# Kernel optimization log

Hardware: AMD Instinct MI355X
Metric: run time of the kernel (lower is better)

Reference implementation:

```python
import jax, jax.numpy as jnp
import numpy as np

N = 16384

def setup_inputs() -> dict:
    key = jax.random.key(0)
    k1, k2 = jax.random.split(key)
    predict = jax.random.normal(k1, (N,), dtype=jnp.float32)
    target = jax.random.normal(k2, (N,), dtype=jnp.float32)
    return {"predict": predict, "target": target}

def reference(predict, target):
    n = predict.shape[0]
    # hardtanh(predict[i]-predict[j]) * hardtanh(target[i]-target[j]) summed over i>j.
    # The product matrix is symmetric with zero diagonal, so the strict lower-
    # triangular sum equals half the full-matrix sum.
    pd = jnp.clip(predict[:, None] - predict[None, :], -1.0, 1.0)  # [N, N]
    td = jnp.clip(target[:, None] - target[None, :], -1.0, 1.0)   # [N, N]
    full_sum = jnp.sum(pd * td)
    num = full_sum * 0.5
    denom = jnp.asarray(n * (n - 1), dtype=predict.dtype)
    return 1.0 - 2.0 * num / denom
```

## Files before the change

### kernel.cpp

```cpp
#include <hip/hip_runtime.h>

#define BLOCK 512
#define IPT   4
#define ITILE 2048
#define JS    128
#define JT_PER_I 16
#define NT    576
#define RBLOCK 1024

typedef _Float16 h2 __attribute__((ext_vector_type(2)));

__global__ __launch_bounds__(BLOCK) void kendall_pairs(
    const float* __restrict__ p, const float* __restrict__ t,
    float* __restrict__ partial, int n) {
    __shared__ unsigned int sjp[JS / 2];
    __shared__ unsigned int sjt[JS / 2];

    const int s = blockIdx.x;
    int bi = (int)((__builtin_sqrtf(4.0f + 2.0f * (float)s) - 2.0f) * 0.25f);
    while (8 * (bi + 1) * (bi + 2) <= s) ++bi;
    while (8 * bi * (bi + 1) > s) --bi;
    const int bj = s - 8 * bi * (bi + 1);
    const float w = (bj < JT_PER_I * bi) ? 2.0f : 1.0f;

    if (threadIdx.x < JS) {
        const int k = threadIdx.x & 63;
        const float2* src = (const float2*)((threadIdx.x < 64 ? p : t) + bj * JS);
        float2 v = src[k];
        h2 hv = {(_Float16)v.x, (_Float16)v.y};
        unsigned int bitsv; __builtin_memcpy(&bitsv, &hv, 4);
        (threadIdx.x < 64 ? sjp : sjt)[k] = bitsv;
    }

    h2 pi2[IPT], ti2[IPT];
#pragma unroll
    for (int u = 0; u < IPT; ++u) {
        int i = bi * ITILE + u * BLOCK + threadIdx.x;
        _Float16 ph = (_Float16)p[i];
        _Float16 th = (_Float16)t[i];
        pi2[u] = (h2){ph, ph};
        ti2[u] = (h2){th, th};
    }
    __syncthreads();

    const h2 neg1 = {(_Float16)-1.0f, (_Float16)-1.0f};
    const h2 pos1 = {(_Float16)1.0f, (_Float16)1.0f};

    float acc[IPT] = {0.0f};
    const uint4* jp4 = (const uint4*)sjp;
    const uint4* jt4 = (const uint4*)sjt;

#pragma unroll 4
    for (int g = 0; g < JS / 8; ++g) {
        uint4 jp = jp4[g];
        uint4 jt = jt4[g];
        unsigned int jpw[4] = {jp.x, jp.y, jp.z, jp.w};
        unsigned int jtw[4] = {jt.x, jt.y, jt.z, jt.w};
#pragma unroll
        for (int c = 0; c < 4; ++c) {
            h2 pj, tj;
            __builtin_memcpy(&pj, &jpw[c], 4);
            __builtin_memcpy(&tj, &jtw[c], 4);
#pragma unroll
            for (int u = 0; u < IPT; ++u) {
                h2 pd = __builtin_elementwise_min(
                            __builtin_elementwise_max(pi2[u] - pj, neg1), pos1);
                h2 td = __builtin_elementwise_min(
                            __builtin_elementwise_max(ti2[u] - tj, neg1), pos1);
                acc[u] = __builtin_amdgcn_fdot2(pd, td, acc[u], false);
            }
        }
    }

    float r = (acc[0] + acc[1]) + (acc[2] + acc[3]);
#pragma unroll
    for (int off = 32; off > 0; off >>= 1) r += __shfl_down(r, off, 64);

    if ((threadIdx.x & 63) == 0)
        partial[blockIdx.x * (BLOCK / 64) + (threadIdx.x >> 6)] = w * r;
}

__global__ __launch_bounds__(RBLOCK) void kendall_reduce(
    const float* __restrict__ partial, float* __restrict__ out,
    int nPartial, int n) {
    __shared__ float wsum[RBLOCK / 64];
    float s = 0.0f;
    for (int k = threadIdx.x; k < nPartial; k += RBLOCK) s += partial[k];
#pragma unroll
    for (int off = 32; off > 0; off >>= 1) s += __shfl_down(s, off, 64);
    const int lane = threadIdx.x & 63;
    const int wid  = threadIdx.x >> 6;
    if (lane == 0) wsum[wid] = s;
    __syncthreads();
    if (threadIdx.x == 0) {
        float S = 0.0f;
#pragma unroll
        for (int v2 = 0; v2 < RBLOCK / 64; ++v2) S += wsum[v2];
        float denom = (float)n * (float)(n - 1);
        out[0] = 1.0f - S / denom;
    }
}

extern "C" void kernel_launch(void* const* d_in, const int* in_sizes, int n_in,
                              void* d_out, int out_size, void* d_ws, size_t ws_size,
                              hipStream_t stream) {
    const float* predict = (const float*)d_in[0];
    const float* target  = (const float*)d_in[1];
    float* out = (float*)d_out;
    float* partial = (float*)d_ws;
    const int n = in_sizes[0];

    const int nPartial = NT * (BLOCK / 64);
    kendall_pairs<<<NT, BLOCK, 0, stream>>>(predict, target, partial, n);
    kendall_reduce<<<1, RBLOCK, 0, stream>>>(partial, out, nPartial, n);
}
```

Measured before the change: 78.31 us.

## Fold hardtanh into packed f16 add with clamp via affine remap

Inputs are remapped so that y = 0.5 + 0.5*(x_i - x_j) is computed with one v_pk_add_f16 using the clamp modifier, which saturates to [0,1]. This replaces the sub/max/min sequence per operand with a single instruction. The final reduction recovers the hardtanh product sum algebraically as S = 4A - n^2, relying on the antisymmetric cross terms cancelling. To get that cancellation the triangular symmetric tiling is dropped for a full N×N grid, which roughly doubles pair work. Occupancy is also hinted through launch bounds. The risks are cancellation error in the fp32 subtraction of n^2 and the reduced fp16 headroom caused by the offset.

New measurement: 70.57 us. -9.9%, faster.

```diff
diff --git a/kernel.cpp b/kernel.cpp
--- a/kernel.cpp
+++ b/kernel.cpp
@@ -4,30 +4,27 @@
 #define IPT   4
 #define ITILE 2048
 #define JS    128
-#define JT_PER_I 16
-#define NT    576
+#define NBI   8
+#define NBJ   128
+#define NT    (NBI * NBJ)
 #define RBLOCK 1024
 
 typedef _Float16 h2 __attribute__((ext_vector_type(2)));
 
-__global__ __launch_bounds__(BLOCK) void kendall_pairs(
+__global__ __launch_bounds__(BLOCK, 8) void kendall_pairs(
     const float* __restrict__ p, const float* __restrict__ t,
     float* __restrict__ partial, int n) {
     __shared__ unsigned int sjp[JS / 2];
     __shared__ unsigned int sjt[JS / 2];
 
-    const int s = blockIdx.x;
-    int bi = (int)((__builtin_sqrtf(4.0f + 2.0f * (float)s) - 2.0f) * 0.25f);
-    while (8 * (bi + 1) * (bi + 2) <= s) ++bi;
-    while (8 * bi * (bi + 1) > s) --bi;
-    const int bj = s - 8 * bi * (bi + 1);
-    const float w = (bj < JT_PER_I * bi) ? 2.0f : 1.0f;
+    const int bi = blockIdx.x >> 7;
+    const int bj = blockIdx.x & (NBJ - 1);
 
     if (threadIdx.x < JS) {
         const int k = threadIdx.x & 63;
         const float2* src = (const float2*)((threadIdx.x < 64 ? p : t) + bj * JS);
         float2 v = src[k];
-        h2 hv = {(_Float16)v.x, (_Float16)v.y};
+        h2 hv = {(_Float16)(0.5f - 0.5f * v.x), (_Float16)(0.5f - 0.5f * v.y)};
         unsigned int bitsv; __builtin_memcpy(&bitsv, &hv, 4);
         (threadIdx.x < 64 ? sjp : sjt)[k] = bitsv;
     }
@@ -36,15 +33,12 @@
 #pragma unroll
     for (int u = 0; u < IPT; ++u) {
         int i = bi * ITILE + u * BLOCK + threadIdx.x;
-        _Float16 ph = (_Float16)p[i];
-        _Float16 th = (_Float16)t[i];
+        _Float16 ph = (_Float16)(0.5f * p[i]);
+        _Float16 th = (_Float16)(0.5f * t[i]);
         pi2[u] = (h2){ph, ph};
         ti2[u] = (h2){th, th};
     }
     __syncthreads();
-
-    const h2 neg1 = {(_Float16)-1.0f, (_Float16)-1.0f};
-    const h2 pos1 = {(_Float16)1.0f, (_Float16)1.0f};
 
     float acc[IPT] = {0.0f};
     const uint4* jp4 = (const uint4*)sjp;
@@ -63,11 +57,10 @@
             __builtin_memcpy(&tj, &jtw[c], 4);
 #pragma unroll
             for (int u = 0; u < IPT; ++u) {
-                h2 pd = __builtin_elementwise_min(
-                            __builtin_elementwise_max(pi2[u] - pj, neg1), pos1);
-                h2 td = __builtin_elementwise_min(
-                            __builtin_elementwise_max(ti2[u] - tj, neg1), pos1);
-                acc[u] = __builtin_amdgcn_fdot2(pd, td, acc[u], false);
+                h2 yp, yt;
+                asm("v_pk_add_f16 %0, %1, %2 clamp" : "=v"(yp) : "v"(pi2[u]), "v"(pj));
+                asm("v_pk_add_f16 %0, %1, %2 clamp" : "=v"(yt) : "v"(ti2[u]), "v"(tj));
+                acc[u] = __builtin_amdgcn_fdot2(yp, yt, acc[u], false);
             }
         }
     }
@@ -77,7 +70,7 @@
     for (int off = 32; off > 0; off >>= 1) r += __shfl_down(r, off, 64);
 
     if ((threadIdx.x & 63) == 0)
-        partial[blockIdx.x * (BLOCK / 64) + (threadIdx.x >> 6)] = w * r;
+        partial[blockIdx.x * (BLOCK / 64) + (threadIdx.x >> 6)] = r;
 }
 
 __global__ __launch_bounds__(RBLOCK) void kendall_reduce(
@@ -93,10 +86,12 @@
     if (lane == 0) wsum[wid] = s;
     __syncthreads();
     if (threadIdx.x == 0) {
-        float S = 0.0f;
+        float A = 0.0f;
 #pragma unroll
-        for (int v2 = 0; v2 < RBLOCK / 64; ++v2) S += wsum[v2];
-        float denom = (float)n * (float)(n - 1);
+        for (int v2 = 0; v2 < RBLOCK / 64; ++v2) A += wsum[v2];
+        float nf = (float)n;
+        float S = 4.0f * A - nf * nf;
+        float denom = nf * (float)(n - 1);
         out[0] = 1.0f - S / denom;
     }
 }
```
